# Performance work log

Measured on AMD Instinct MI355X. Metric: run time of the kernel, lower is better.

The kernel has to match this reference:

```python
import jax, jax.numpy as jnp
import numpy as np

B, S, D = 8, 2048, 1024
NEG = -1000000000.0  # float32 masking constant from original code


def setup_inputs() -> dict:
    key = jax.random.key(0)
    kq, kk, kv, km = jax.random.split(key, 4)
    q = jax.random.normal(kq, (B, S, D), dtype=jnp.float32)
    k = jax.random.normal(kk, (B, S, D), dtype=jnp.float32)
    v = jax.random.normal(kv, (B, S, D), dtype=jnp.float32)
    mask = (jax.random.uniform(km, (B, 1, S)) < 0.1).astype(jnp.float32)
    return {"q": q, "k": k, "v": v, "mask": mask}


def reference(q, k, v, mask):
    scale = jnp.asarray(D ** -0.5, dtype=q.dtype)
    # [B,S,S] = q @ k^T, scaled
    logits = jnp.einsum("bqd,bkd->bqk", q, k) * scale
    logits = logits + mask * NEG  # mask broadcasts over query axis
    attn = jax.nn.softmax(logits, axis=-1)
    return jnp.einsum("bqk,bkd->bqd", attn, v)
```

## Files before the change

### kernel.cpp

```cpp
#include <hip/hip_runtime.h>
#include <hip/hip_bf16.h>

#define NB 8
#define SS 2048
#define DDIM 1024

typedef __attribute__((ext_vector_type(8))) short bf16x8;
typedef __attribute__((ext_vector_type(4))) float f32x4;

__device__ inline void gload_lds16(const void* g, void* l) {
  __builtin_amdgcn_global_load_lds(
      (const __attribute__((address_space(1))) void*)g,
      (__attribute__((address_space(3))) void*)l, 16, 0, 0);
}

__device__ inline ushort f2bf(float f) {
  union { float f; unsigned int u; } v;
  v.f = f;
  unsigned int u = v.u;
  unsigned int r = (u + 0x7FFFu + ((u >> 16) & 1u)) >> 16;
  return (ushort)r;
}

__device__ inline unsigned int pack2(float a, float b) {
  return (unsigned int)f2bf(a) | ((unsigned int)f2bf(b) << 16);
}

__global__ void init_zero(float* __restrict__ p, int n) {
  int i = blockIdx.x * 256 + threadIdx.x;
  if (i < n) p[i] = 0.f;
}

__global__ void conv_bf16(const float* __restrict__ in, ushort* __restrict__ out,
                          int n8) {
  int i = blockIdx.x * 256 + threadIdx.x;
  if (i >= n8) return;
  const float4* p = (const float4*)in + (size_t)i * 2;
  float4 a = p[0], b = p[1];
  uint4 o;
  o.x = pack2(a.x, a.y);
  o.y = pack2(a.z, a.w);
  o.z = pack2(b.x, b.y);
  o.w = pack2(b.z, b.w);
  ((uint4*)out)[i] = o;
}

__global__ void conv_transpose_v(const float* __restrict__ V,
                                 ushort* __restrict__ VT) {
  __shared__ ushort tile[64][65];
  const int b = blockIdx.z;
  const int k0 = blockIdx.x * 64;
  const int d0 = blockIdx.y * 64;
  const float* Vb = V + (size_t)b * SS * DDIM;
  ushort* VTb = VT + (size_t)b * DDIM * SS;
  const int t = threadIdx.x;
#pragma unroll
  for (int i = 0; i < 4; i++) {
    int j = i * 256 + t;
    int r = j >> 4, cg = j & 15;
    float4 f = *(const float4*)(Vb + (size_t)(k0 + r) * DDIM + d0 + cg * 4);
    tile[r][cg * 4 + 0] = f2bf(f.x);
    tile[r][cg * 4 + 1] = f2bf(f.y);
    tile[r][cg * 4 + 2] = f2bf(f.z);
    tile[r][cg * 4 + 3] = f2bf(f.w);
  }
  __syncthreads();
#pragma unroll
  for (int i = 0; i < 2; i++) {
    int j = i * 256 + t;
    int r = j >> 3, cg = j & 7;
    ushort u[8];
#pragma unroll
    for (int u8 = 0; u8 < 8; u8++) u[u8] = tile[cg * 8 + u8][r];
    *(uint4*)(VTb + (size_t)(d0 + r) * SS + k0 + cg * 8) = *(uint4*)u;
  }
}

#define MFMA16(mh, nh, BF)                                                    \
  _Pragma("unroll") for (int ks = 0; ks < 2; ks++)                            \
  _Pragma("unroll") for (int mi = 0; mi < 4; mi++)                            \
  _Pragma("unroll") for (int ni = 0; ni < 2; ni++)                            \
      acc[mh][mi][nh][ni] = __builtin_amdgcn_mfma_f32_16x16x32_bf16(          \
          af[mi][ks], BF[ni][ks], acc[mh][mi][nh][ni], 0, 0, 0);

#define PHASE(mh, nh, BF)                                                     \
  __builtin_amdgcn_s_barrier();                                               \
  asm volatile("s_waitcnt lgkmcnt(0)" ::: "memory");                          \
  __builtin_amdgcn_sched_barrier(0);                                          \
  __builtin_amdgcn_s_setprio(1);                                              \
  MFMA16(mh, nh, BF);                                                         \
  __builtin_amdgcn_s_setprio(0);                                              \
  __builtin_amdgcn_sched_barrier(0);

#define VMW(n) asm volatile("s_waitcnt vmcnt(" #n ")" ::: "memory")
#define LGK8 asm volatile("s_waitcnt lgkmcnt(8)" ::: "memory")
#define ENDP() __builtin_amdgcn_s_barrier()

#define RD_A(d, h)                                                            \
  _Pragma("unroll") for (int mi = 0; mi < 4; mi++) {                          \
    const char* _p = ldsc + (d) * 65536 + (h) * 16384 + aoff[mi];             \
    af[mi][0] = *(const bf16x8*)(_p + koff0);                                 \
    af[mi][1] = *(const bf16x8*)(_p + koff1);                                 \
  }

#define RD_B(d, h, dst)                                                       \
  _Pragma("unroll") for (int ni = 0; ni < 2; ni++) {                          \
    const char* _p = ldsc + (d) * 65536 + 32768 + (h) * 16384 + boff[ni];     \
    dst[ni][0] = *(const bf16x8*)(_p + koff0);                                \
    dst[ni][1] = *(const bf16x8*)(_p + koff1);                                \
  }

#define STAGE(dbuf, isB, h, kt_)                                              \
  do {                                                                        \
    const ushort* _s = (isB) ? Bb : Ab;                                       \
    const int _t0 = (isB) ? tileN : tileM;                                    \
    char* _lb = ldsc + (dbuf) * 65536 + (isB) * 32768 + (h) * 16384;          \
    gload_lds16(_s + (size_t)(_t0 + (h) * 128 + r0) * K + (kt_) * 64 + c8,    \
                _lb + ol0);                                                   \
    gload_lds16(_s + (size_t)(_t0 + (h) * 128 + r1) * K + (kt_) * 64 + c8,    \
                _lb + ol1);                                                   \
  } while (0)

template <bool EXPEPI, typename OutT>
__global__ __launch_bounds__(512, 2) void gemm_bt(
    const ushort* __restrict__ A, const ushort* __restrict__ Bm,
    OutT* __restrict__ C, const float* __restrict__ maskp,
    float* __restrict__ rowsum, int M, int N, int K, float alpha) {
  __shared__ __attribute__((aligned(128))) char ldsc[131072];
  const int tid = threadIdx.x;
  const int wave = tid >> 6, lane = tid & 63;
  const int quad = lane >> 4, l16 = lane & 15;
  const int wm = wave >> 2, wn = wave & 3;

  const int gx = gridDim.x, gy = gridDim.y;
  const int lin = blockIdx.x + gx * (blockIdx.y + gy * blockIdx.z);
  const int nwg = gx * gy * (int)gridDim.z;
  const int cpx = nwg >> 3;
  const int swz = (lin & 7) * cpx + (lin >> 3);
  const int bz = swz / (gx * gy);
  const int rem = swz - bz * (gx * gy);
  const int by = rem / gx;
  const int bx = rem - by * gx;

  const int b = bz;
  const ushort* Ab = A + (size_t)b * M * K;
  const ushort* Bb = Bm + (size_t)b * N * K;
  const int tileM = by * 256, tileN = bx * 256;

  const int ol0 = wave * 2048 + lane * 16;
  const int ol1 = ol0 + 1024;
  const int r0 = ol0 >> 7;
  const int r1 = r0 + 8;
  const int c8 = (((lane & 7) ^ (r0 & 7)) * 8);

  const int x7 = lane & 7;
  const int koff0 = ((quad) ^ x7) * 16;
  const int koff1 = ((4 + quad) ^ x7) * 16;
  int aoff[4], boff[2];
#pragma unroll
  for (int mi = 0; mi < 4; mi++) aoff[mi] = (wm * 64 + mi * 16 + l16) * 128;
#pragma unroll
  for (int ni = 0; ni < 2; ni++) boff[ni] = (wn * 32 + ni * 16 + l16) * 128;

  f32x4 acc[2][4][2][2];
#pragma unroll
  for (int mh = 0; mh < 2; mh++)
#pragma unroll
    for (int mi = 0; mi < 4; mi++)
#pragma unroll
      for (int nh = 0; nh < 2; nh++)
#pragma unroll
        for (int ni = 0; ni < 2; ni++)
          acc[mh][mi][nh][ni] = (f32x4){0.f, 0.f, 0.f, 0.f};

  bf16x8 af[4][2], bfa[2][2], bfb[2][2];
  const int NKT = K >> 6;
  const int NIT = NKT >> 1;

  STAGE(0, 0, 0, 0);
  STAGE(0, 1, 0, 0);
  STAGE(0, 1, 1, 0);
  STAGE(0, 0, 1, 0);
  STAGE(1, 0, 0, 1);
  STAGE(1, 1, 0, 1);
  STAGE(1, 1, 1, 1);
  VMW(6);
  __builtin_amdgcn_s_barrier();

  for (int it = 0; it < NIT - 1; ++it) {
    const int tb = 2 * it;
    RD_A(0, 0); RD_B(0, 0, bfa); STAGE(1, 0, 1, tb + 1); LGK8;
    PHASE(0, 0, bfa); ENDP();
    RD_B(0, 1, bfb); STAGE(0, 0, 0, tb + 2);
    PHASE(0, 1, bfb); ENDP();
    RD_A(0, 1); STAGE(0, 1, 0, tb + 2);
    PHASE(1, 1, bfb); ENDP();
    STAGE(0, 1, 1, tb + 2);
    PHASE(1, 0, bfa); VMW(6); ENDP();
    RD_A(1, 0); RD_B(1, 0, bfa); STAGE(0, 0, 1, tb + 2); LGK8;
    PHASE(0, 0, bfa); ENDP();
    RD_B(1, 1, bfb); STAGE(1, 0, 0, tb + 3);
    PHASE(0, 1, bfb); ENDP();
    RD_A(1, 1); STAGE(1, 1, 0, tb + 3);
    PHASE(1, 1, bfb); ENDP();
    STAGE(1, 1, 1, tb + 3);
    PHASE(1, 0, bfa); VMW(6); ENDP();
  }
  {
    RD_A(0, 0); RD_B(0, 0, bfa); STAGE(1, 0, 1, NKT - 1); LGK8;
    PHASE(0, 0, bfa); ENDP();
    RD_B(0, 1, bfb);
    PHASE(0, 1, bfb); ENDP();
    RD_A(0, 1);
    PHASE(1, 1, bfb); ENDP();
    PHASE(1, 0, bfa); VMW(0); ENDP();
    RD_A(1, 0); RD_B(1, 0, bfa);
    PHASE(0, 0, bfa); ENDP();
    RD_B(1, 1, bfb);
    PHASE(0, 1, bfb); ENDP();
    RD_A(1, 1);
    PHASE(1, 1, bfb); ENDP();
    PHASE(1, 0, bfa);
  }

  OutT* Cb = C + (size_t)b * M * N;
  if (EXPEPI) {
    const float* mb = maskp + (size_t)b * N;
    float mv[2][2];
#pragma unroll
    for (int nh = 0; nh < 2; nh++)
#pragma unroll
      for (int ni = 0; ni < 2; ni++)
        mv[nh][ni] = mb[tileN + nh * 128 + wn * 32 + ni * 16 + l16] * (-1e9f);
#pragma unroll
    for (int mh = 0; mh < 2; mh++)
#pragma unroll
    for (int mi = 0; mi < 4; mi++) {
#pragma unroll
      for (int rr = 0; rr < 4; rr++) {
        const int row = tileM + mh * 128 + wm * 64 + mi * 16 + quad * 4 + rr;
        float s = 0.f;
#pragma unroll
        for (int nh = 0; nh < 2; nh++)
#pragma unroll
        for (int ni = 0; ni < 2; ni++) {
          const int col = tileN + nh * 128 + wn * 32 + ni * 16 + l16;
          float e = __expf(acc[mh][mi][nh][ni][rr] * alpha + mv[nh][ni]);
          ((ushort*)Cb)[(size_t)row * N + col] = f2bf(e);
          s += e;
        }
        s += __shfl_xor(s, 1, 64);
        s += __shfl_xor(s, 2, 64);
        s += __shfl_xor(s, 4, 64);
        s += __shfl_xor(s, 8, 64);
        if (l16 == 0) atomicAdd(&rowsum[(size_t)b * M + row], s);
      }
    }
  } else {
#pragma unroll
    for (int mh = 0; mh < 2; mh++)
#pragma unroll
    for (int mi = 0; mi < 4; mi++) {
      float inv[4];
#pragma unroll
      for (int rr = 0; rr < 4; rr++) {
        const int row = tileM + mh * 128 + wm * 64 + mi * 16 + quad * 4 + rr;
        inv[rr] = 1.0f / rowsum[(size_t)b * M + row];
      }
#pragma unroll
      for (int nh = 0; nh < 2; nh++)
#pragma unroll
      for (int ni = 0; ni < 2; ni++) {
        const int col = tileN + nh * 128 + wn * 32 + ni * 16 + l16;
#pragma unroll
        for (int rr = 0; rr < 4; rr++) {
          const int row = tileM + mh * 128 + wm * 64 + mi * 16 + quad * 4 + rr;
          ((float*)Cb)[(size_t)row * N + col] =
              acc[mh][mi][nh][ni][rr] * alpha * inv[rr];
        }
      }
    }
  }
}

extern "C" void kernel_launch(void* const* d_in, const int* in_sizes, int n_in,
                              void* d_out, int out_size, void* d_ws, size_t ws_size,
                              hipStream_t stream) {
  const float* q = (const float*)d_in[0];
  const float* k = (const float*)d_in[1];
  const float* v = (const float*)d_in[2];
  const float* mask = (const float*)d_in[3];
  float* out = (float*)d_out;

  const size_t pQ = (size_t)SS * DDIM * 2;
  const size_t pP = (size_t)SS * SS * 2;
  const size_t pR = (size_t)SS * 4;

  int gb = 8;
  while (gb > 1 && (size_t)gb * (3 * pQ + pP + pR) > ws_size) gb >>= 1;

  for (int b0 = 0; b0 < NB; b0 += gb) {
    char* w = (char*)d_ws;
    ushort* qb = (ushort*)w;
    ushort* kb = (ushort*)(w + (size_t)gb * pQ);
    ushort* vtb = (ushort*)(w + (size_t)gb * pQ * 2);
    ushort* Sc = (ushort*)(w + (size_t)gb * pQ * 3);
    float* rowsum = (float*)(w + (size_t)gb * (pQ * 3 + pP));

    const float* qg = q + (size_t)b0 * SS * DDIM;
    const float* kg = k + (size_t)b0 * SS * DDIM;
    const float* vg = v + (size_t)b0 * SS * DDIM;
    const float* mg = mask + (size_t)b0 * SS;
    float* og = out + (size_t)b0 * SS * DDIM;

    const int nrs = gb * SS;
    init_zero<<<(nrs + 255) / 256, 256, 0, stream>>>(rowsum, nrs);
    const int n8 = gb * SS * DDIM / 8;
    conv_bf16<<<n8 / 256, 256, 0, stream>>>(qg, qb, n8);
    conv_bf16<<<n8 / 256, 256, 0, stream>>>(kg, kb, n8);
    conv_transpose_v<<<dim3(SS / 64, DDIM / 64, gb), 256, 0, stream>>>(vg, vtb);
    gemm_bt<true, ushort><<<dim3(SS / 256, SS / 256, gb), 512, 0, stream>>>(
        qb, kb, Sc, mg, rowsum, SS, SS, DDIM, 0.03125f);
    gemm_bt<false, float><<<dim3(DDIM / 256, SS / 256, gb), 512, 0, stream>>>(
        Sc, vtb, og, nullptr, rowsum, SS, DDIM, SS, 1.0f);
  }
}
```

Measured before the change: 389.6 us.

## Use single B-fragment register set with reordered staging; merge Q/K conversion launches

The GEMM main loop drops the second B-fragment register set: each phase now reloads its B fragment from LDS into one buffer, so the order in which LDS halves are staged and freed is reshuffled to match. This frees VGPRs to help sustain two 512-thread blocks per CU, at the cost of extra LDS reads per iteration and tighter ordering between stage writes and fragment reads. Separately, the Q and K fp32-to-bf16 conversions are merged into one launch over a 2D grid to save a kernel launch.

```diff
diff --git a/kernel.cpp b/kernel.cpp
--- a/kernel.cpp
+++ b/kernel.cpp
@@ -31,10 +31,14 @@
   if (i < n) p[i] = 0.f;
 }
 
-__global__ void conv_bf16(const float* __restrict__ in, ushort* __restrict__ out,
-                          int n8) {
+__global__ void conv_bf16_qk(const float* __restrict__ qin,
+                             const float* __restrict__ kin,
+                             ushort* __restrict__ qout,
+                             ushort* __restrict__ kout, int n8) {
   int i = blockIdx.x * 256 + threadIdx.x;
   if (i >= n8) return;
+  const float* in = blockIdx.y ? kin : qin;
+  ushort* out = blockIdx.y ? kout : qout;
   const float4* p = (const float4*)in + (size_t)i * 2;
   float4 a = p[0], b = p[1];
   uint4 o;
@@ -76,19 +80,19 @@
   }
 }
 
-#define MFMA16(mh, nh, BF)                                                    \
+#define MFMA16(mh, nh)                                                        \
   _Pragma("unroll") for (int ks = 0; ks < 2; ks++)                            \
   _Pragma("unroll") for (int mi = 0; mi < 4; mi++)                            \
   _Pragma("unroll") for (int ni = 0; ni < 2; ni++)                            \
       acc[mh][mi][nh][ni] = __builtin_amdgcn_mfma_f32_16x16x32_bf16(          \
-          af[mi][ks], BF[ni][ks], acc[mh][mi][nh][ni], 0, 0, 0);
-
-#define PHASE(mh, nh, BF)                                                     \
+          af[mi][ks], bf[ni][ks], acc[mh][mi][nh][ni], 0, 0, 0);
+
+#define PHASE(mh, nh)                                                         \
   __builtin_amdgcn_s_barrier();                                               \
   asm volatile("s_waitcnt lgkmcnt(0)" ::: "memory");                          \
   __builtin_amdgcn_sched_barrier(0);                                          \
   __builtin_amdgcn_s_setprio(1);                                              \
-  MFMA16(mh, nh, BF);                                                         \
+  MFMA16(mh, nh);                                                             \
   __builtin_amdgcn_s_setprio(0);                                              \
   __builtin_amdgcn_sched_barrier(0);
 
@@ -103,11 +107,11 @@
     af[mi][1] = *(const bf16x8*)(_p + koff1);                                 \
   }
 
-#define RD_B(d, h, dst)                                                       \
+#define RD_B(d, h)                                                            \
   _Pragma("unroll") for (int ni = 0; ni < 2; ni++) {                          \
     const char* _p = ldsc + (d) * 65536 + 32768 + (h) * 16384 + boff[ni];     \
-    dst[ni][0] = *(const bf16x8*)(_p + koff0);                                \
-    dst[ni][1] = *(const bf16x8*)(_p + koff1);                                \
+    bf[ni][0] = *(const bf16x8*)(_p + koff0);                                 \
+    bf[ni][1] = *(const bf16x8*)(_p + koff1);                                 \
   }
 
 #define STAGE(dbuf, isB, h, kt_)                                              \
@@ -173,7 +177,7 @@
         for (int ni = 0; ni < 2; ni++)
           acc[mh][mi][nh][ni] = (f32x4){0.f, 0.f, 0.f, 0.f};
 
-  bf16x8 af[4][2], bfa[2][2], bfb[2][2];
+  bf16x8 af[4][2], bf[2][2];
   const int NKT = K >> 6;
   const int NIT = NKT >> 1;
 
@@ -182,45 +186,47 @@
   STAGE(0, 1, 1, 0);
   STAGE(0, 0, 1, 0);
   STAGE(1, 0, 0, 1);
-  STAGE(1, 1, 0, 1);
   STAGE(1, 1, 1, 1);
+  STAGE(1, 0, 1, 1);
   VMW(6);
   __builtin_amdgcn_s_barrier();
 
   for (int it = 0; it < NIT - 1; ++it) {
     const int tb = 2 * it;
-    RD_A(0, 0); RD_B(0, 0, bfa); STAGE(1, 0, 1, tb + 1); LGK8;
-    PHASE(0, 0, bfa); ENDP();
-    RD_B(0, 1, bfb); STAGE(0, 0, 0, tb + 2);
-    PHASE(0, 1, bfb); ENDP();
-    RD_A(0, 1); STAGE(0, 1, 0, tb + 2);
-    PHASE(1, 1, bfb); ENDP();
-    STAGE(0, 1, 1, tb + 2);
-    PHASE(1, 0, bfa); VMW(6); ENDP();
-    RD_A(1, 0); RD_B(1, 0, bfa); STAGE(0, 0, 1, tb + 2); LGK8;
-    PHASE(0, 0, bfa); ENDP();
-    RD_B(1, 1, bfb); STAGE(1, 0, 0, tb + 3);
-    PHASE(0, 1, bfb); ENDP();
-    RD_A(1, 1); STAGE(1, 1, 0, tb + 3);
-    PHASE(1, 1, bfb); ENDP();
-    STAGE(1, 1, 1, tb + 3);
-    PHASE(1, 0, bfa); VMW(6); ENDP();
+    RD_A(0, 0); RD_B(0, 0); STAGE(1, 1, 0, tb + 1); LGK8;
+    PHASE(0, 0); ENDP();
+    RD_B(0, 1); STAGE(0, 0, 0, tb + 2);
+    PHASE(0, 1); ENDP();
+    RD_A(0, 1); STAGE(0, 1, 1, tb + 2);
+    PHASE(1, 1); ENDP();
+    RD_B(0, 0); STAGE(0, 0, 1, tb + 2);
+    PHASE(1, 0); VMW(6); ENDP();
+    RD_A(1, 0); RD_B(1, 0); STAGE(0, 1, 0, tb + 2); LGK8;
+    PHASE(0, 0); ENDP();
+    RD_B(1, 1); STAGE(1, 0, 0, tb + 3);
+    PHASE(0, 1); ENDP();
+    RD_A(1, 1); STAGE(1, 1, 1, tb + 3);
+    PHASE(1, 1); ENDP();
+    RD_B(1, 0); STAGE(1, 0, 1, tb + 3);
+    PHASE(1, 0); VMW(6); ENDP();
   }
   {
-    RD_A(0, 0); RD_B(0, 0, bfa); STAGE(1, 0, 1, NKT - 1); LGK8;
-    PHASE(0, 0, bfa); ENDP();
-    RD_B(0, 1, bfb);
-    PHASE(0, 1, bfb); ENDP();
+    RD_A(0, 0); RD_B(0, 0); STAGE(1, 1, 0, NKT - 1); LGK8;
+    PHASE(0, 0); ENDP();
+    RD_B(0, 1);
+    PHASE(0, 1); ENDP();
     RD_A(0, 1);
-    PHASE(1, 1, bfb); ENDP();
-    PHASE(1, 0, bfa); VMW(0); ENDP();
-    RD_A(1, 0); RD_B(1, 0, bfa);
-    PHASE(0, 0, bfa); ENDP();
-    RD_B(1, 1, bfb);
-    PHASE(0, 1, bfb); ENDP();
+    PHASE(1, 1); ENDP();
+    RD_B(0, 0);
+    PHASE(1, 0); VMW(0); ENDP();
+    RD_A(1, 0); RD_B(1, 0); LGK8;
+    PHASE(0, 0); ENDP();
+    RD_B(1, 1);
+    PHASE(0, 1); ENDP();
     RD_A(1, 1);
-    PHASE(1, 1, bfb); ENDP();
-    PHASE(1, 0, bfa);
+    PHASE(1, 1); ENDP();
+    RD_B(1, 0);
+    PHASE(1, 0);
   }
 
   OutT* Cb = C + (size_t)b * M * N;
@@ -316,8 +322,7 @@
     const int nrs = gb * SS;
     init_zero<<<(nrs + 255) / 256, 256, 0, stream>>>(rowsum, nrs);
     const int n8 = gb * SS * DDIM / 8;
-    conv_bf16<<<n8 / 256, 256, 0, stream>>>(qg, qb, n8);
-    conv_bf16<<<n8 / 256, 256, 0, stream>>>(kg, kb, n8);
+    conv_bf16_qk<<<dim3(n8 / 256, 2), 256, 0, stream>>>(qg, kg, qb, kb, n8);
     conv_transpose_v<<<dim3(SS / 64, DDIM / 64, gb), 256, 0, stream>>>(vg, vtb);
     gemm_bt<true, ushort><<<dim3(SS / 256, SS / 256, gb), 512, 0, stream>>>(
         qb, kb, Sc, mg, rowsum, SS, SS, DDIM, 0.03125f);
```

Measured after the change: 367.0 us. -5.8%, faster.
